# Kernel tuning notes

Hardware: AMD Instinct MI355X
Metric: run time of the kernel (lower is better)

Reference implementation:

```python
import math
import jax, jax.numpy as jnp
import numpy as np

B, L, C, H = 4, 2048, 1024, 16
D = C // H  # head dim = 64

def setup_inputs() -> dict:
    key = jax.random.key(0)
    k1, k2, k3 = jax.random.split(key, 3)
    x = jax.random.normal(k1, (B, L, C), dtype=jnp.float32)
    w_attn = jax.random.normal(k2, (C, 3 * C), dtype=jnp.float32) * (1.0 / math.sqrt(C))
    w_proj = jax.random.normal(k3, (C, C), dtype=jnp.float32) * (1.0 / math.sqrt(C))
    return {"x": x, "w_attn": w_attn, "w_proj": w_proj}

def reference(x, w_attn, w_proj):
    b, l, c = x.shape
    s = x @ w_attn                      # (B,L,3C)
    q, k, v = s[:, :, :c], s[:, :, c:2 * c], s[:, :, 2 * c:]
    # (B,L,H,D) -> (B,H,L,D)
    q = q.reshape(b, l, H, D).transpose(0, 2, 1, 3)
    k = k.reshape(b, l, H, D).transpose(0, 2, 1, 3)
    v = v.reshape(b, l, H, D).transpose(0, 2, 1, 3)
    att = jnp.einsum('bhqd,bhkd->bhqk', q, k) * (1.0 / math.sqrt(D))
    causal = jnp.tril(jnp.ones((l, l), dtype=bool))
    att = jnp.where(causal[None, None], att, -jnp.inf)
    att = jax.nn.softmax(att, axis=-1)
    y = jnp.einsum('bhqk,bhkd->bhqd', att, v)
    y = y.transpose(0, 2, 1, 3).reshape(b, l, c)
    return y @ w_proj
```

## Files before the change

kernel.cpp:

```cpp
#include <hip/hip_runtime.h>
#include <math.h>

typedef unsigned short u16;
typedef unsigned int u32;
typedef __bf16 bf16x8 __attribute__((ext_vector_type(8)));
typedef float f32x4 __attribute__((ext_vector_type(4)));
typedef float f32x16 __attribute__((ext_vector_type(16)));
typedef u16 u16x4 __attribute__((ext_vector_type(4)));
typedef u16 u16x8 __attribute__((ext_vector_type(8)));
typedef u32 u32x4 __attribute__((ext_vector_type(4)));

#define MFMA16(a, b, c) __builtin_amdgcn_mfma_f32_16x16x32_bf16((a), (b), (c), 0, 0, 0)
#define MFMA32(a, b, c) __builtin_amdgcn_mfma_f32_32x32x16_bf16((a), (b), (c), 0, 0, 0)

#define GLL16(g, l)                                                   \
  __builtin_amdgcn_global_load_lds(                                   \
      (const __attribute__((address_space(1))) void*)(g),             \
      (__attribute__((address_space(3))) void*)(l), 16, 0, 0)

__device__ __forceinline__ u16 f2bf(float f) {
  __bf16 h = (__bf16)f;
  return __builtin_bit_cast(u16, h);
}
__device__ __forceinline__ u32 pack2(float a, float b) {
  return (u32)f2bf(a) | ((u32)f2bf(b) << 16);
}

__global__ __launch_bounds__(256) void cvt_f32_bf16(const float* __restrict__ in,
                                                    u16* __restrict__ out) {
  size_t i = ((size_t)blockIdx.x * 256 + threadIdx.x) * 4;
  float4 v = *(const float4*)(in + i);
  u16x4 o;
  o[0] = f2bf(v.x); o[1] = f2bf(v.y); o[2] = f2bf(v.z); o[3] = f2bf(v.w);
  *(u16x4*)(out + i) = o;
}

__global__ __launch_bounds__(256) void transpose_w(const float* __restrict__ in,
                                                   u16* __restrict__ out,
                                                   int R, int Cn) {
  __shared__ u16 tile[64][72];
  const int t = threadIdx.x;
  const int tr = blockIdx.y * 64;
  const int tc = blockIdx.x * 64;
#pragma unroll
  for (int p = 0; p < 4; ++p) {
    int chunk = p * 256 + t;
    int r = chunk >> 4, cq = chunk & 15;
    float4 v = *(const float4*)(in + (size_t)(tr + r) * Cn + tc + cq * 4);
    tile[r][cq * 4 + 0] = f2bf(v.x);
    tile[r][cq * 4 + 1] = f2bf(v.y);
    tile[r][cq * 4 + 2] = f2bf(v.z);
    tile[r][cq * 4 + 3] = f2bf(v.w);
  }
  __syncthreads();
#pragma unroll
  for (int p = 0; p < 2; ++p) {
    int chunk = p * 256 + t;
    int c = chunk >> 3, rg = chunk & 7;
    u16x8 v;
#pragma unroll
    for (int i = 0; i < 8; ++i) v[i] = tile[rg * 8 + i][c];
    *(u16x8*)(out + (size_t)(tc + c) * R + tr + rg * 8) = v;
  }
}

__global__ __launch_bounds__(256) void transpose_v(const u16* __restrict__ S,
                                                   u16* __restrict__ VT) {
  __shared__ u16 tile[64][72];
  const int t = threadIdx.x;
  const int lt = blockIdx.x;
  const int bh = blockIdx.y;
  const int b = bh >> 4, h = bh & 15;
  const u16* src = S + ((size_t)b * 2048 + (size_t)lt * 64) * 3072 + 2048 + h * 64;
  u16* dst = VT + (size_t)bh * 64 * 2048 + (size_t)lt * 64;
#pragma unroll
  for (int p = 0; p < 2; ++p) {
    int chunk = p * 256 + t;
    int r = chunk >> 3, cg = chunk & 7;
    u16x8 v = *(const u16x8*)(src + (size_t)r * 3072 + cg * 8);
    *(u16x8*)(&tile[r][cg * 8]) = v;
  }
  __syncthreads();
#pragma unroll
  for (int p = 0; p < 2; ++p) {
    int chunk = p * 256 + t;
    int d = chunk >> 3, rg = chunk & 7;
    u16x8 v;
#pragma unroll
    for (int i = 0; i < 8; ++i) v[i] = tile[rg * 8 + i][d];
    *(u16x8*)(dst + (size_t)d * 2048 + rg * 8) = v;
  }
}

template <bool OUTF32>
__global__ __launch_bounds__(256, 2) void gemm_bt(const u16* __restrict__ A,
                                                  const u16* __restrict__ BT,
                                                  void* __restrict__ Cp,
                                                  int M, int N, int K) {
  __shared__ u16 As[128 * 64];
  __shared__ u16 Bs[128 * 64];
  const int tid = threadIdx.x;
  const int lane = tid & 63;
  const int wid = tid >> 6;
  const int wr = wid >> 1, wc = wid & 1;
  const int rl = lane & 15, kg = lane >> 4;
  const size_t rowA0 = (size_t)blockIdx.y * 128;
  const size_t rowB0 = (size_t)blockIdx.x * 128;

  const int r_st = tid >> 3;
  const int cg_st = tid & 7;

  f32x4 acc[4][4] = {};

  for (int kb = 0; kb < K; kb += 64) {
    __syncthreads();
#pragma unroll
    for (int it = 0; it < 4; ++it) {
      int r = it * 32 + r_st;
      int cgs = cg_st ^ (r & 7);
      GLL16(A + (rowA0 + r) * K + kb + cgs * 8, As + (size_t)r * 64 + cg_st * 8);
      GLL16(BT + (rowB0 + r) * K + kb + cgs * 8, Bs + (size_t)r * 64 + cg_st * 8);
    }
    __syncthreads();

    bf16x8 af[2][4], bfr[2][4];
#pragma unroll
    for (int kk = 0; kk < 2; ++kk) {
      int c8 = kk * 4 + kg;
#pragma unroll
      for (int m = 0; m < 4; ++m) {
        int ra = wr * 64 + m * 16 + rl;
        af[kk][m] = *(const bf16x8*)(As + (size_t)ra * 64 + (size_t)((c8 ^ (ra & 7)) * 8));
        int rb = wc * 64 + m * 16 + rl;
        bfr[kk][m] = *(const bf16x8*)(Bs + (size_t)rb * 64 + (size_t)((c8 ^ (rb & 7)) * 8));
      }
    }
#pragma unroll
    for (int kk = 0; kk < 2; ++kk)
#pragma unroll
      for (int m = 0; m < 4; ++m)
#pragma unroll
        for (int n = 0; n < 4; ++n)
          acc[m][n] = MFMA16(af[kk][m], bfr[kk][n], acc[m][n]);
  }

#pragma unroll
  for (int m = 0; m < 4; ++m)
#pragma unroll
    for (int n = 0; n < 4; ++n)
#pragma unroll
      for (int j = 0; j < 4; ++j) {
        size_t r = rowA0 + wr * 64 + m * 16 + kg * 4 + j;
        size_t c = rowB0 + wc * 64 + n * 16 + rl;
        if constexpr (OUTF32)
          ((float*)Cp)[r * N + c] = acc[m][n][j];
        else
          ((u16*)Cp)[r * N + c] = f2bf(acc[m][n][j]);
      }
}

__global__ __launch_bounds__(256) void attn(const u16* __restrict__ S,
                                            const u16* __restrict__ VT,
                                            u16* __restrict__ Y) {
  __shared__ u16 Ks[2][64 * 64];
  __shared__ u16 Vs[2][64 * 64];
  const int g = blockIdx.x;
  const int t1 = 31 - g;
  const int bh = blockIdx.y;
  const int b = bh >> 4, h = bh & 15;
  const int tid = threadIdx.x, lane = tid & 63, wid = tid >> 6;
  const int ql = lane & 31;
  const int hi = lane >> 5;
  const int grp = wid >> 1;
  const int hw = wid & 1;
  const int myt = grp ? t1 : g;
  const int qrow = myt * 64 + hw * 32 + ql;

  const u16* Sq = S + (size_t)b * 2048 * 3072 + h * 64;
  const u16* Sk = Sq + 1024;
  const u16* Vh = VT + (size_t)bh * 64 * 2048;

  const int sr = tid >> 3, scg = tid & 7;

#define STAGE(buf, kt)                                                          \
  {                                                                             \
    _Pragma("unroll") for (int it = 0; it < 2; ++it) {                          \
      int r = it * 32 + sr;                                                     \
      int cs = scg ^ (r & 7);               \
      GLL16(Sk + (size_t)((kt) * 64 + r) * 3072 + cs * 8,                       \
            &Ks[buf][r * 64 + scg * 8]);                                        \
      GLL16(Vh + (size_t)r * 2048 + (kt) * 64 + cs * 8,                         \
            &Vs[buf][r * 64 + scg * 8]);                                        \
    }                                                                           \
  }

  const float SC = 0.125f * 1.44269504088896f;
  bf16x8 qf[4];
#pragma unroll
  for (int s4 = 0; s4 < 4; ++s4) {
    bf16x8 q = *(const bf16x8*)(Sq + (size_t)qrow * 3072 + s4 * 16 + hi * 8);
    bf16x8 qs;
#pragma unroll
    for (int i = 0; i < 8; ++i) qs[i] = (__bf16)((float)q[i] * SC);
    qf[s4] = qs;
  }

  f32x16 O0 = {}, O1 = {};
  float mj = -INFINITY, lj = 0.f;

  STAGE(0, 0);
  __syncthreads();

  for (int kt = 0; kt <= t1; ++kt) {
    const int cur = kt & 1;
    if (kt < t1) STAGE(cur ^ 1, kt + 1);
    const u16* Ksb = Ks[cur];
    const u16* Vsb = Vs[cur];

    const bool active = (grp == 1) || (kt <= g);
    if (active) {
      f32x16 s0 = {}, s1 = {};
      __builtin_amdgcn_s_setprio(1);
#pragma unroll
      for (int s4 = 0; s4 < 4; ++s4) {
        int cix = (2 * s4 + hi) ^ (ql & 7);
        bf16x8 kf0 = *(const bf16x8*)(Ksb + (size_t)ql * 64 + cix * 8);
        bf16x8 kf1 = *(const bf16x8*)(Ksb + (size_t)(32 + ql) * 64 + cix * 8);
        s0 = MFMA32(kf0, qf[s4], s0);
        s1 = MFMA32(kf1, qf[s4], s1);
      }
      __builtin_amdgcn_s_setprio(0);

      if (kt == myt) {
        const int lim = hw * 32 + ql;
#pragma unroll
        for (int r = 0; r < 16; ++r) {
          int c0 = (r & 3) + 8 * (r >> 2) + 4 * hi;
          s0[r] = (c0 <= lim) ? s0[r] : -INFINITY;
          s1[r] = (32 + c0 <= lim) ? s1[r] : -INFINITY;
        }
      }

      float t16[16];
#pragma unroll
      for (int r = 0; r < 16; ++r) t16[r] = fmaxf(s0[r], s1[r]);
#pragma unroll
      for (int off = 8; off >= 1; off >>= 1)
#pragma unroll
        for (int i = 0; i < 8; ++i)
          if (i < off) t16[i] = fmaxf(t16[i], t16[i + off]);
      float rmax = fmaxf(t16[0], __shfl_xor(t16[0], 32));
      float mn = fmaxf(mj, rmax);
      float scl = exp2f(mj - mn);
      mj = mn;
#pragma unroll
      for (int r = 0; r < 16; ++r) {
        s0[r] = exp2f(s0[r] - mn);
        s1[r] = exp2f(s1[r] - mn);
      }
      float a16[16];
#pragma unroll
      for (int r = 0; r < 16; ++r) a16[r] = s0[r] + s1[r];
#pragma unroll
      for (int off = 8; off >= 1; off >>= 1)
#pragma unroll
        for (int i = 0; i < 8; ++i)
          if (i < off) a16[i] += a16[i + off];
      float rsum = a16[0] + __shfl_xor(a16[0], 32);
      lj = lj * scl + rsum;
#pragma unroll
      for (int r = 0; r < 16; ++r) { O0[r] *= scl; O1[r] *= scl; }

      __builtin_amdgcn_s_setprio(1);
#pragma unroll
      for (int Sstep = 0; Sstep < 4; ++Sstep) {
        const int kb = Sstep >> 1, s = Sstep & 1;
        float e0 = kb ? s1[8 * s + 0] : s0[8 * s + 0];
        float e1 = kb ? s1[8 * s + 1] : s0[8 * s + 1];
        float e2 = kb ? s1[8 * s + 2] : s0[8 * s + 2];
        float e3 = kb ? s1[8 * s + 3] : s0[8 * s + 3];
        float f0 = kb ? s1[8 * s + 4] : s0[8 * s + 4];
        float f1 = kb ? s1[8 * s + 5] : s0[8 * s + 5];
        float f2 = kb ? s1[8 * s + 6] : s0[8 * s + 6];
        float f3 = kb ? s1[8 * s + 7] : s0[8 * s + 7];
        u32 a0 = pack2(e0, e1), a1 = pack2(e2, e3);
        u32 b0 = pack2(f0, f1), b1 = pack2(f2, f3);
        u32 s0w = hi ? a0 : b0;
        u32 s1w = hi ? a1 : b1;
        u32 r0 = (u32)__shfl_xor((int)s0w, 32);
        u32 r1 = (u32)__shfl_xor((int)s1w, 32);
        u32x4 pw;
        pw[0] = hi ? r0 : a0;
        pw[1] = hi ? r1 : a1;
        pw[2] = hi ? b0 : r0;
        pw[3] = hi ? b1 : r1;
        bf16x8 pf = __builtin_bit_cast(bf16x8, pw);
        int cix = (2 * Sstep + hi) ^ (ql & 7);
        bf16x8 vf0 = *(const bf16x8*)(Vsb + (size_t)ql * 64 + cix * 8);
        bf16x8 vf1 = *(const bf16x8*)(Vsb + (size_t)(32 + ql) * 64 + cix * 8);
        O0 = MFMA32(vf0, pf, O0);
        O1 = MFMA32(vf1, pf, O1);
      }
      __builtin_amdgcn_s_setprio(0);
    }
    __syncthreads();
  }

  const float inv = 1.0f / lj;
  u16* yrow = Y + (size_t)(b * 2048 + qrow) * 1024 + h * 64;
#pragma unroll
  for (int db = 0; db < 2; ++db)
#pragma unroll
    for (int rq = 0; rq < 4; ++rq) {
      u16x4 o;
#pragma unroll
      for (int j = 0; j < 4; ++j) {
        float v = (db ? O1[rq * 4 + j] : O0[rq * 4 + j]) * inv;
        o[j] = f2bf(v);
      }
      *(u16x4*)(yrow + db * 32 + 8 * rq + 4 * hi) = o;
    }
#undef STAGE
}

extern "C" void kernel_launch(void* const* d_in, const int* in_sizes, int n_in,
                              void* d_out, int out_size, void* d_ws, size_t ws_size,
                              hipStream_t stream) {
  const float* x = (const float*)d_in[0];
  const float* w_attn = (const float*)d_in[1];
  const float* w_proj = (const float*)d_in[2];
  float* out = (float*)d_out;

  u16* S = (u16*)d_ws;
  u16* WT1 = S + (size_t)8192 * 3072;
  u16* WT2 = WT1 + (size_t)3072 * 1024;
  u16* VT = WT2 + (size_t)1024 * 1024;
  u16* Y = VT + (size_t)64 * 64 * 2048;
  u16* XB = Y + (size_t)8192 * 1024;

  cvt_f32_bf16<<<8192, 256, 0, stream>>>(x, XB);
  transpose_w<<<dim3(3072 / 64, 1024 / 64), 256, 0, stream>>>(w_attn, WT1, 1024, 3072);
  transpose_w<<<dim3(1024 / 64, 1024 / 64), 256, 0, stream>>>(w_proj, WT2, 1024, 1024);
  gemm_bt<false><<<dim3(3072 / 128, 8192 / 128), 256, 0, stream>>>(XB, WT1, S, 8192, 3072, 1024);
  transpose_v<<<dim3(32, 64), 256, 0, stream>>>(S, VT);
  attn<<<dim3(16, 64), 256, 0, stream>>>(S, VT, Y);
  gemm_bt<true><<<dim3(1024 / 128, 8192 / 128), 256, 0, stream>>>(Y, WT2, out, 8192, 1024, 1024);
}
```

Baseline: 343.5 us.

## Lazy softmax rescale, raw v_exp, XCD block swizzle in GEMM, reorder attention grid

The attention kernel now rescales the running max and accumulators only when some lane's max grows by more than a threshold (8 in log2 units), which skips most rescale multiplies. It also calls v_exp_f32 directly through inline asm in place of exp2f. The GEMM remaps block IDs so consecutive blocks land on the same XCD chunk for better L2 reuse, and the attention grid is transposed so heads vary fastest. The lazy rescale lets values grow up to 2^8 before renormalising, which costs some precision headroom, and raw v_exp drops exp2f's denormal and range handling.

```diff
diff --git a/kernel.cpp b/kernel.cpp
--- a/kernel.cpp
+++ b/kernel.cpp
@@ -24,6 +24,11 @@
 }
 __device__ __forceinline__ u32 pack2(float a, float b) {
   return (u32)f2bf(a) | ((u32)f2bf(b) << 16);
+}
+__device__ __forceinline__ float exp2a(float x) {
+  float r;
+  asm("v_exp_f32 %0, %1" : "=v"(r) : "v"(x));
+  return r;
 }
 
 __global__ __launch_bounds__(256) void cvt_f32_bf16(const float* __restrict__ in,
@@ -104,8 +109,14 @@
   const int wid = tid >> 6;
   const int wr = wid >> 1, wc = wid & 1;
   const int rl = lane & 15, kg = lane >> 4;
-  const size_t rowA0 = (size_t)blockIdx.y * 128;
-  const size_t rowB0 = (size_t)blockIdx.x * 128;
+
+  const int id = blockIdx.x + gridDim.x * blockIdx.y;
+  const int cpx = (gridDim.x * gridDim.y) >> 3;
+  const int swz = (id & 7) * cpx + (id >> 3);
+  const int bx = swz % gridDim.x;
+  const int by = swz / gridDim.x;
+  const size_t rowA0 = (size_t)by * 128;
+  const size_t rowB0 = (size_t)bx * 128;
 
   const int r_st = tid >> 3;
   const int cg_st = tid & 7;
@@ -164,9 +175,9 @@
                                             u16* __restrict__ Y) {
   __shared__ u16 Ks[2][64 * 64];
   __shared__ u16 Vs[2][64 * 64];
-  const int g = blockIdx.x;
+  const int bh = blockIdx.x;
+  const int g = blockIdx.y;
   const int t1 = 31 - g;
-  const int bh = blockIdx.y;
   const int b = bh >> 4, h = bh & 15;
   const int tid = threadIdx.x, lane = tid & 63, wid = tid >> 6;
   const int ql = lane & 31;
@@ -250,13 +261,20 @@
         for (int i = 0; i < 8; ++i)
           if (i < off) t16[i] = fmaxf(t16[i], t16[i + off]);
       float rmax = fmaxf(t16[0], __shfl_xor(t16[0], 32));
-      float mn = fmaxf(mj, rmax);
-      float scl = exp2f(mj - mn);
-      mj = mn;
+
+      if (__any(rmax > mj + 8.0f)) {
+        float mn = (rmax > mj + 8.0f) ? rmax : mj;
+        float scl = exp2a(mj - mn);
+        mj = mn;
+        lj *= scl;
+#pragma unroll
+        for (int r = 0; r < 16; ++r) { O0[r] *= scl; O1[r] *= scl; }
+      }
+
 #pragma unroll
       for (int r = 0; r < 16; ++r) {
-        s0[r] = exp2f(s0[r] - mn);
-        s1[r] = exp2f(s1[r] - mn);
+        s0[r] = exp2a(s0[r] - mj);
+        s1[r] = exp2a(s1[r] - mj);
       }
       float a16[16];
 #pragma unroll
@@ -266,10 +284,7 @@
 #pragma unroll
         for (int i = 0; i < 8; ++i)
           if (i < off) a16[i] += a16[i + off];
-      float rsum = a16[0] + __shfl_xor(a16[0], 32);
-      lj = lj * scl + rsum;
-#pragma unroll
-      for (int r = 0; r < 16; ++r) { O0[r] *= scl; O1[r] *= scl; }
+      lj += a16[0] + __shfl_xor(a16[0], 32);
 
       __builtin_amdgcn_s_setprio(1);
 #pragma unroll
@@ -343,6 +358,6 @@
   transpose_w<<<dim3(1024 / 64, 1024 / 64), 256, 0, stream>>>(w_proj, WT2, 1024, 1024);
   gemm_bt<false><<<dim3(3072 / 128, 8192 / 128), 256, 0, stream>>>(XB, WT1, S, 8192, 3072, 1024);
   transpose_v<<<dim3(32, 64), 256, 0, stream>>>(S, VT);
-  attn<<<dim3(16, 64), 256, 0, stream>>>(S, VT, Y);
+  attn<<<dim3(64, 16), 256, 0, stream>>>(S, VT, Y);
   gemm_bt<true><<<dim3(1024 / 128, 8192 / 128), 256, 0, stream>>>(Y, WT2, out, 8192, 1024, 1024);
 }
```

Measured after the change: 286.9 us. 16.5% less time.
